# Performance work log

Measured on AMD Instinct MI355X. Metric: run time of the kernel, lower is better.

## Reference

```python
import jax, jax.numpy as jnp
import numpy as np

ROUTINGS = 3
NUM_CAPSULES = 16


def squash(s, eps=1e-8):
    # s: [..., dim_capsule]
    norm = jnp.linalg.norm(s, axis=-1, keepdims=True)
    return (norm ** 2) / (1.0 + norm ** 2) * (s / (norm + eps))


def setup_inputs() -> dict:
    key = jax.random.key(0)
    k1, k2 = jax.random.split(key)
    x = jax.random.normal(k1, (64, 1024, 64), dtype=jnp.float32)      # [B, n_in, input_dim]
    weight = jax.random.normal(k2, (16, 64, 32), dtype=jnp.float32)    # [nc, input_dim, dc]
    return {"x": x, "weight": weight}


def reference(x, weight):
    B, n_in, _ = x.shape
    nc = weight.shape[0]
    # prediction vectors u_hat: [B, nc, n_in, dc]
    u_hat = jnp.einsum('bni,cid->bcnd', x, weight)
    # routing logits, softmax taken over the output-capsule axis (dim=1 in torch)
    b = jnp.zeros((B, nc, n_in, 1), dtype=u_hat.dtype)
    v = None
    for i in range(ROUTINGS):
        c = jax.nn.softmax(b, axis=1)                 # [B, nc, n_in, 1]
        s = jnp.sum(c * u_hat, axis=2)                # [B, nc, dc]
        v = squash(s)                                 # [B, nc, dc]
        if i < ROUTINGS - 1:
            # agreement: <u_hat, v> per input capsule
            b = b + jnp.einsum('bcnd,bcd->bcn', u_hat, v)[..., None]
    return v
```

## Files before the change

### kernel.cpp

```cpp
#include <hip/hip_runtime.h>
#include <math.h>

#define B_SZ 64
#define N_IN 1024
#define IDIM 64
#define NC   16
#define DC   32
#define NQ   4
#define QR   256
#define NTHR 1024
#define XS   68
#define AS   20

#define WS_CS  0
#define WS_SP1 16384
#define WS_SP2 278528
#define WS_WV0 540672

__device__ __forceinline__ float rdlane_f(float v, int l) {
    return __int_as_float(__builtin_amdgcn_readlane(__float_as_int(v), l));
}


__device__ __forceinline__ void stage_x(const float* __restrict__ x, float* xT,
                                        int b, int q, int tid) {
    const float4* xb4 = reinterpret_cast<const float4*>(x + ((size_t)b * N_IN + q * QR) * IDIM);
#pragma unroll
    for (int m = 0; m < 4; m++) {
        const int f = tid + m * NTHR;
        const float4 v4 = xb4[f];
        const int n = f >> 4, i0 = (f & 15) * 4;
        *reinterpret_cast<float4*>(&xT[n * XS + i0]) = v4;
    }
}

__device__ __forceinline__ float route_pass(const float* xT, const float* wSm,
                                            float* aSmT, float* pSm,
                                            int tid, int lane, int wave,
                                            int row, int grp, int rq) {
    const float4 wr4 = *reinterpret_cast<const float4*>(&wSm[lane * AS + grp * 4]);
    {
        float a0 = 0.f, a1 = 0.f, a2 = 0.f, a3 = 0.f;
#pragma unroll
        for (int iq = 0; iq < 16; iq++) {
            const float4 xv = *reinterpret_cast<const float4*>(&xT[row * XS + iq * 4]);
#pragma unroll
            for (int j = 0; j < 4; j++) {
                const int i = iq * 4 + j;
                const float xc = (j == 0) ? xv.x : (j == 1) ? xv.y
                               : (j == 2) ? xv.z : xv.w;
                a0 += rdlane_f(wr4.x, i) * xc;
                a1 += rdlane_f(wr4.y, i) * xc;
                a2 += rdlane_f(wr4.z, i) * xc;
                a3 += rdlane_f(wr4.w, i) * xc;
            }
        }
        *reinterpret_cast<float4*>(&aSmT[row * AS + grp * 4]) =
            make_float4(a0, a1, a2, a3);
    }
    __syncthreads();
    float cw0, cw1, cw2, cw3;
    {
        const float4 q0 = *reinterpret_cast<const float4*>(&aSmT[row * AS + 0]);
        const float4 q1 = *reinterpret_cast<const float4*>(&aSmT[row * AS + 4]);
        const float4 q2 = *reinterpret_cast<const float4*>(&aSmT[row * AS + 8]);
        const float4 q3 = *reinterpret_cast<const float4*>(&aSmT[row * AS + 12]);
        float av[NC] = {q0.x, q0.y, q0.z, q0.w, q1.x, q1.y, q1.z, q1.w,
                        q2.x, q2.y, q2.z, q2.w, q3.x, q3.y, q3.z, q3.w};
        float mx = av[0];
#pragma unroll
        for (int k = 1; k < NC; k++) mx = fmaxf(mx, av[k]);
        float ss = 0.f;
#pragma unroll
        for (int k = 0; k < NC; k++) { av[k] = __expf(av[k] - mx); ss += av[k]; }
        const float inv = 1.f / ss;
        if (grp == 0)      { cw0 = av[0];  cw1 = av[1];  cw2 = av[2];  cw3 = av[3];  }
        else if (grp == 1) { cw0 = av[4];  cw1 = av[5];  cw2 = av[6];  cw3 = av[7];  }
        else if (grp == 2) { cw0 = av[8];  cw1 = av[9];  cw2 = av[10]; cw3 = av[11]; }
        else               { cw0 = av[12]; cw1 = av[13]; cw2 = av[14]; cw3 = av[15]; }
        cw0 *= inv; cw1 *= inv; cw2 *= inv; cw3 *= inv;
    }
    {
        float s0 = 0.f, s1 = 0.f, s2 = 0.f, s3 = 0.f;
#pragma unroll
        for (int nl = 0; nl < 64; nl++) {
            const float xv = xT[(rq * 64 + nl) * XS + lane];
            s0 += rdlane_f(cw0, nl) * xv;
            s1 += rdlane_f(cw1, nl) * xv;
            s2 += rdlane_f(cw2, nl) * xv;
            s3 += rdlane_f(cw3, nl) * xv;
        }
        *reinterpret_cast<float4*>(&pSm[(rq * 64 + lane) * AS + grp * 4]) =
            make_float4(s0, s1, s2, s3);
    }
    __syncthreads();
    return pSm[(0 * 64 + lane) * AS + wave] + pSm[(1 * 64 + lane) * AS + wave] +
           pSm[(2 * 64 + lane) * AS + wave] + pSm[(3 * 64 + lane) * AS + wave];
}

__device__ __forceinline__ void caps_sv(const float* __restrict__ W, const float* redSm,
                                        float* vSm, int tid, bool modeRed0, bool toOut,
                                        float* __restrict__ outp, int b) {
    if (tid < 512) {
        const int c = tid >> 5, dd = tid & 31;
        const float* Wc = W + c * (IDIM * DC) + dd;
        float s = 0.f;
#pragma unroll 8
        for (int i = 0; i < IDIM; i++) {
            const float rv = modeRed0 ? redSm[i] : redSm[c * 64 + i];
            s += rv * Wc[i * DC];
        }
        if (modeRed0) s *= 0.0625f;
        float n2 = s * s;
#pragma unroll
        for (int m = 16; m >= 1; m >>= 1) n2 += __shfl_xor(n2, m);
        const float g = (n2 / (1.f + n2)) / (sqrtf(n2) + 1e-8f);
        if (toOut) outp[b * (NC * DC) + c * DC + dd] = g * s;
        else       vSm[c * 36 + dd] = g * s;
    }
    __syncthreads();
}

__device__ __forceinline__ float caps_wv(const float* __restrict__ W, const float* vSm,
                                         int tid) {
    const int i = tid >> 4, c = tid & 15;
    const float4* Wr = reinterpret_cast<const float4*>(W + (size_t)(c * IDIM + i) * DC);
    const float4* vv = reinterpret_cast<const float4*>(&vSm[c * 36]);
    float acc = 0.f;
#pragma unroll
    for (int dq = 0; dq < 8; dq++) {
        const float4 wq = Wr[dq], vq = vv[dq];
        acc += wq.x * vq.x + wq.y * vq.y + wq.z * vq.z + wq.w * vq.w;
    }
    return acc;
}

__global__ __launch_bounds__(256) void k_colsum(const float* __restrict__ x,
                                                float* __restrict__ cs) {
    const int b = blockIdx.y, q = blockIdx.x;
    const int tid = threadIdx.x;
    const float4* xb4 = reinterpret_cast<const float4*>(x + ((size_t)b * N_IN + q * QR) * IDIM);
    float4 s4 = {0.f, 0.f, 0.f, 0.f};
#pragma unroll
    for (int m = 0; m < 16; m++) {
        const float4 v4 = xb4[tid + m * 256];
        s4.x += v4.x; s4.y += v4.y; s4.z += v4.z; s4.w += v4.w;
    }
    __shared__ float red[16][64];
    const int g = tid >> 4, i0 = (tid & 15) * 4;
    red[g][i0 + 0] = s4.x; red[g][i0 + 1] = s4.y;
    red[g][i0 + 2] = s4.z; red[g][i0 + 3] = s4.w;
    __syncthreads();
    if (tid < 64) {
        float r = 0.f;
#pragma unroll
        for (int k = 0; k < 16; k++) r += red[k][tid];
        cs[(b * NQ + q) * 64 + tid] = r;
    }
}

__global__ __launch_bounds__(NTHR, 1)
void k_iter1(const float* __restrict__ x, const float* __restrict__ W,
             const float* __restrict__ cs, float* __restrict__ sp1,
             float* __restrict__ wv0) {
    const int b = blockIdx.x & 63, q = blockIdx.x >> 6;
    const int tid = threadIdx.x, lane = tid & 63, wave = tid >> 6;
    const int row = tid & 255, grp = tid >> 8, rq = wave & 3;

    __shared__ float __align__(16) xT[QR * XS];
    __shared__ float __align__(16) aSmT[QR * AS];
    __shared__ float __align__(16) pSm[4 * 64 * AS];
    __shared__ float __align__(16) wSm[IDIM * AS];
    __shared__ float redSm[NC * IDIM];
    __shared__ float __align__(16) vSm[NC * 36];

    stage_x(x, xT, b, q, tid);
    if (tid < 64) {
        float r = 0.f;
#pragma unroll
        for (int k = 0; k < NQ; k++) r += cs[(b * NQ + k) * 64 + tid];
        redSm[tid] = r;
    }
    __syncthreads();
    caps_sv(W, redSm, vSm, tid, true, false, nullptr, b);
    {
        const float acc = caps_wv(W, vSm, tid);
        wSm[(tid >> 4) * AS + (tid & 15)] = acc;
        if (q == 0) wv0[b * 1024 + tid] = acc;
    }
    __syncthreads();
    const float val = route_pass(xT, wSm, aSmT, pSm, tid, lane, wave, row, grp, rq);
    sp1[(size_t)(b * NQ + q) * 1024 + tid] = val;
}

__global__ __launch_bounds__(NTHR, 1)
void k_iter2(const float* __restrict__ x, const float* __restrict__ W,
             const float* __restrict__ sp1, float* __restrict__ sp2,
             const float* __restrict__ wv0) {
    const int b = blockIdx.x & 63, q = blockIdx.x >> 6;
    const int tid = threadIdx.x, lane = tid & 63, wave = tid >> 6;
    const int row = tid & 255, grp = tid >> 8, rq = wave & 3;

    __shared__ float __align__(16) xT[QR * XS];
    __shared__ float __align__(16) aSmT[QR * AS];
    __shared__ float __align__(16) pSm[4 * 64 * AS];
    __shared__ float __align__(16) wSm[IDIM * AS];
    __shared__ float redSm[NC * IDIM];
    __shared__ float __align__(16) vSm[NC * 36];

    stage_x(x, xT, b, q, tid);
    {
        float r = 0.f;
#pragma unroll
        for (int k = 0; k < NQ; k++) r += sp1[(size_t)(b * NQ + k) * 1024 + tid];
        redSm[tid] = r;
    }
    __syncthreads();
    caps_sv(W, redSm, vSm, tid, false, false, nullptr, b);
    wSm[(tid >> 4) * AS + (tid & 15)] = caps_wv(W, vSm, tid) + wv0[b * 1024 + tid];
    __syncthreads();
    const float val = route_pass(xT, wSm, aSmT, pSm, tid, lane, wave, row, grp, rq);
    sp2[(size_t)(b * NQ + q) * 1024 + tid] = val;
}

__global__ __launch_bounds__(NTHR) void k_final(const float* __restrict__ sp2,
                                                const float* __restrict__ W,
                                                float* __restrict__ out) {
    const int b = blockIdx.x, tid = threadIdx.x;
    __shared__ float redSm[NC * IDIM];
    __shared__ float __align__(16) vSm[NC * 36];
    {
        float r = 0.f;
#pragma unroll
        for (int k = 0; k < NQ; k++) r += sp2[(size_t)(b * NQ + k) * 1024 + tid];
        redSm[tid] = r;
    }
    __syncthreads();
    caps_sv(W, redSm, vSm, tid, false, true, out, b);
}

extern "C" void kernel_launch(void* const* d_in, const int* in_sizes, int n_in,
                              void* d_out, int out_size, void* d_ws, size_t ws_size,
                              hipStream_t stream) {
    const float* x = (const float*)d_in[0];
    const float* W = (const float*)d_in[1];
    float* out = (float*)d_out;
    float* ws = (float*)d_ws;

    float* cs  = ws + WS_CS;
    float* sp1 = ws + WS_SP1;
    float* sp2 = ws + WS_SP2;
    float* wv0 = ws + WS_WV0;

    k_colsum<<<dim3(NQ, B_SZ), 256, 0, stream>>>(x, cs);
    k_iter1<<<B_SZ * NQ, NTHR, 0, stream>>>(x, W, cs, sp1, wv0);
    k_iter2<<<B_SZ * NQ, NTHR, 0, stream>>>(x, W, sp1, sp2, wv0);
    k_final<<<B_SZ, NTHR, 0, stream>>>(sp2, W, out);
}
```

Measured before the change: 43.99 us.

## Split routing kernels into 8 chunks of 128 rows with 512-thread blocks

Halves the rows handled per block (128 instead of 256) and the threads per block (512 instead of 1024). This doubles the grid of the two routing kernels to 512 blocks and allows up to 4 blocks per CU. Each thread now produces two partial outputs and computes two halves of the W·v product, and the partial-sum buffers grow to 8 chunks. The aim is better CU occupancy and more parallelism on a GPU with many CUs. The cost is more partial sums to reduce and the per-block setup (caps_sv and W·v) being repeated across twice as many blocks.

```diff
diff --git a/kernel.cpp b/kernel.cpp
--- a/kernel.cpp
+++ b/kernel.cpp
@@ -6,16 +6,17 @@
 #define IDIM 64
 #define NC   16
 #define DC   32
-#define NQ   4
-#define QR   256
-#define NTHR 1024
+#define NQ0  4
+#define NQ   8
+#define QR   128
+#define NTHR 512
 #define XS   68
 #define AS   20
 
 #define WS_CS  0
 #define WS_SP1 16384
-#define WS_SP2 278528
-#define WS_WV0 540672
+#define WS_SP2 540672
+#define WS_WV0 1064960
 
 __device__ __forceinline__ float rdlane_f(float v, int l) {
     return __int_as_float(__builtin_amdgcn_readlane(__float_as_int(v), l));
@@ -34,10 +35,11 @@
     }
 }
 
-__device__ __forceinline__ float route_pass(const float* xT, const float* wSm,
-                                            float* aSmT, float* pSm,
-                                            int tid, int lane, int wave,
-                                            int row, int grp, int rq) {
+__device__ __forceinline__ void route_pass(const float* xT, const float* wSm,
+                                           float* aSmT, float* pSm,
+                                           int tid, int lane, int wave,
+                                           int row, int grp, int rq,
+                                           float& vA, float& vB) {
     const float4 wr4 = *reinterpret_cast<const float4*>(&wSm[lane * AS + grp * 4]);
     {
         float a0 = 0.f, a1 = 0.f, a2 = 0.f, a3 = 0.f;
@@ -94,8 +96,9 @@
             make_float4(s0, s1, s2, s3);
     }
     __syncthreads();
-    return pSm[(0 * 64 + lane) * AS + wave] + pSm[(1 * 64 + lane) * AS + wave] +
-           pSm[(2 * 64 + lane) * AS + wave] + pSm[(3 * 64 + lane) * AS + wave];
+    const int io = tid & 63, co = tid >> 6;
+    vA = pSm[io * AS + co]       + pSm[(64 + io) * AS + co];
+    vB = pSm[io * AS + (co + 8)] + pSm[(64 + io) * AS + (co + 8)];
 }
 
 __device__ __forceinline__ void caps_sv(const float* __restrict__ W, const float* redSm,
@@ -121,9 +124,9 @@
     __syncthreads();
 }
 
-__device__ __forceinline__ float caps_wv(const float* __restrict__ W, const float* vSm,
-                                         int tid) {
-    const int i = tid >> 4, c = tid & 15;
+__device__ __forceinline__ float caps_wv_h(const float* __restrict__ W, const float* vSm,
+                                           int tid, int h) {
+    const int i = (tid >> 4) + 32 * h, c = tid & 15;
     const float4* Wr = reinterpret_cast<const float4*>(W + (size_t)(c * IDIM + i) * DC);
     const float4* vv = reinterpret_cast<const float4*>(&vSm[c * 36]);
     float acc = 0.f;
@@ -139,7 +142,7 @@
                                                 float* __restrict__ cs) {
     const int b = blockIdx.y, q = blockIdx.x;
     const int tid = threadIdx.x;
-    const float4* xb4 = reinterpret_cast<const float4*>(x + ((size_t)b * N_IN + q * QR) * IDIM);
+    const float4* xb4 = reinterpret_cast<const float4*>(x + ((size_t)b * N_IN + q * 256) * IDIM);
     float4 s4 = {0.f, 0.f, 0.f, 0.f};
 #pragma unroll
     for (int m = 0; m < 16; m++) {
@@ -155,21 +158,21 @@
         float r = 0.f;
 #pragma unroll
         for (int k = 0; k < 16; k++) r += red[k][tid];
-        cs[(b * NQ + q) * 64 + tid] = r;
-    }
-}
-
-__global__ __launch_bounds__(NTHR, 1)
+        cs[(b * NQ0 + q) * 64 + tid] = r;
+    }
+}
+
+__global__ __launch_bounds__(NTHR, 4)
 void k_iter1(const float* __restrict__ x, const float* __restrict__ W,
              const float* __restrict__ cs, float* __restrict__ sp1,
              float* __restrict__ wv0) {
     const int b = blockIdx.x & 63, q = blockIdx.x >> 6;
     const int tid = threadIdx.x, lane = tid & 63, wave = tid >> 6;
-    const int row = tid & 255, grp = tid >> 8, rq = wave & 3;
+    const int row = tid & 127, grp = tid >> 7, rq = wave & 1;
 
     __shared__ float __align__(16) xT[QR * XS];
     __shared__ float __align__(16) aSmT[QR * AS];
-    __shared__ float __align__(16) pSm[4 * 64 * AS];
+    __shared__ float __align__(16) pSm[QR * AS];
     __shared__ float __align__(16) wSm[IDIM * AS];
     __shared__ float redSm[NC * IDIM];
     __shared__ float __align__(16) vSm[NC * 36];
@@ -178,52 +181,70 @@
     if (tid < 64) {
         float r = 0.f;
 #pragma unroll
-        for (int k = 0; k < NQ; k++) r += cs[(b * NQ + k) * 64 + tid];
+        for (int k = 0; k < NQ0; k++) r += cs[(b * NQ0 + k) * 64 + tid];
         redSm[tid] = r;
     }
     __syncthreads();
     caps_sv(W, redSm, vSm, tid, true, false, nullptr, b);
-    {
-        const float acc = caps_wv(W, vSm, tid);
-        wSm[(tid >> 4) * AS + (tid & 15)] = acc;
-        if (q == 0) wv0[b * 1024 + tid] = acc;
-    }
-    __syncthreads();
-    const float val = route_pass(xT, wSm, aSmT, pSm, tid, lane, wave, row, grp, rq);
-    sp1[(size_t)(b * NQ + q) * 1024 + tid] = val;
-}
-
-__global__ __launch_bounds__(NTHR, 1)
+#pragma unroll
+    for (int h = 0; h < 2; h++) {
+        const float acc = caps_wv_h(W, vSm, tid, h);
+        const int i = (tid >> 4) + 32 * h, c = tid & 15;
+        wSm[i * AS + c] = acc;
+        if (q == 0) wv0[b * 1024 + tid + h * 512] = acc;
+    }
+    __syncthreads();
+    float vA, vB;
+    route_pass(xT, wSm, aSmT, pSm, tid, lane, wave, row, grp, rq, vA, vB);
+    float* spq = sp1 + (size_t)(b * NQ + q) * 1024;
+    spq[tid] = vA;
+    spq[tid + 512] = vB;
+}
+
+__global__ __launch_bounds__(NTHR, 4)
 void k_iter2(const float* __restrict__ x, const float* __restrict__ W,
              const float* __restrict__ sp1, float* __restrict__ sp2,
              const float* __restrict__ wv0) {
     const int b = blockIdx.x & 63, q = blockIdx.x >> 6;
     const int tid = threadIdx.x, lane = tid & 63, wave = tid >> 6;
-    const int row = tid & 255, grp = tid >> 8, rq = wave & 3;
+    const int row = tid & 127, grp = tid >> 7, rq = wave & 1;
 
     __shared__ float __align__(16) xT[QR * XS];
     __shared__ float __align__(16) aSmT[QR * AS];
-    __shared__ float __align__(16) pSm[4 * 64 * AS];
+    __shared__ float __align__(16) pSm[QR * AS];
     __shared__ float __align__(16) wSm[IDIM * AS];
     __shared__ float redSm[NC * IDIM];
     __shared__ float __align__(16) vSm[NC * 36];
 
     stage_x(x, xT, b, q, tid);
     {
-        float r = 0.f;
-#pragma unroll
-        for (int k = 0; k < NQ; k++) r += sp1[(size_t)(b * NQ + k) * 1024 + tid];
-        redSm[tid] = r;
+        float r0 = 0.f, r1 = 0.f;
+#pragma unroll
+        for (int k = 0; k < NQ; k++) {
+            const float* s = sp1 + (size_t)(b * NQ + k) * 1024;
+            r0 += s[tid];
+            r1 += s[tid + 512];
+        }
+        redSm[tid] = r0;
+        redSm[tid + 512] = r1;
     }
     __syncthreads();
     caps_sv(W, redSm, vSm, tid, false, false, nullptr, b);
-    wSm[(tid >> 4) * AS + (tid & 15)] = caps_wv(W, vSm, tid) + wv0[b * 1024 + tid];
-    __syncthreads();
-    const float val = route_pass(xT, wSm, aSmT, pSm, tid, lane, wave, row, grp, rq);
-    sp2[(size_t)(b * NQ + q) * 1024 + tid] = val;
-}
-
-__global__ __launch_bounds__(NTHR) void k_final(const float* __restrict__ sp2,
+#pragma unroll
+    for (int h = 0; h < 2; h++) {
+        const float acc = caps_wv_h(W, vSm, tid, h);
+        const int i = (tid >> 4) + 32 * h, c = tid & 15;
+        wSm[i * AS + c] = acc + wv0[b * 1024 + tid + h * 512];
+    }
+    __syncthreads();
+    float vA, vB;
+    route_pass(xT, wSm, aSmT, pSm, tid, lane, wave, row, grp, rq, vA, vB);
+    float* spq = sp2 + (size_t)(b * NQ + q) * 1024;
+    spq[tid] = vA;
+    spq[tid + 512] = vB;
+}
+
+__global__ __launch_bounds__(1024) void k_final(const float* __restrict__ sp2,
                                                 const float* __restrict__ W,
                                                 float* __restrict__ out) {
     const int b = blockIdx.x, tid = threadIdx.x;
@@ -252,8 +273,8 @@
     float* sp2 = ws + WS_SP2;
     float* wv0 = ws + WS_WV0;
 
-    k_colsum<<<dim3(NQ, B_SZ), 256, 0, stream>>>(x, cs);
+    k_colsum<<<dim3(NQ0, B_SZ), 256, 0, stream>>>(x, cs);
     k_iter1<<<B_SZ * NQ, NTHR, 0, stream>>>(x, W, cs, sp1, wv0);
     k_iter2<<<B_SZ * NQ, NTHR, 0, stream>>>(x, W, sp1, sp2, wv0);
-    k_final<<<B_SZ, NTHR, 0, stream>>>(sp2, W, out);
-}
+    k_final<<<B_SZ, 1024, 0, stream>>>(sp2, W, out);
+}
```

After: 49.72 us. +13.0%, slower.
